# Kernel tuning notes

Hardware: AMD Instinct MI355X
Metric: run time of the kernel (lower is better)

## Reference

```python
import jax, jax.numpy as jnp
import numpy as np

POOL = 7  # adaptive_avg_pool2d output size (7,7)


def _bin_edges(start, length):
    """Adaptive-avg-pool bin boundaries.
    start, length: [N] int32 -> (lo, hi) each [N, POOL] absolute indices,
    matching torch: lo_i = floor(i*L/P), hi_i = ceil((i+1)*L/P).
    """
    i = jnp.arange(POOL, dtype=jnp.int32)
    lo = start[:, None] + (i[None, :] * length[:, None]) // POOL
    hi = start[:, None] + (-((-(i[None, :] + 1)) * length[:, None] // POOL))
    # note: ceil(a/b) = -(-a // b); written below explicitly
    hi = start[:, None] - ((-(i[None, :] + 1) * length[:, None]) // POOL)
    return lo, hi


def roi_adaptive_avg_pool(features, rois):
    """features: [1, C, H, W]; rois: [N, 4] int (x1,y1,x2,y2 inclusive).
    Returns [N, C, POOL, POOL] == torch stack of adaptive_avg_pool2d over
    features[:, :, y1:y2+1, x1:x2+1], vectorized via an integral image.
    """
    B, C, H, W = features.shape  # B == 1 (forced by shared_fcs input dim)
    # integral image with a zero row/col prepended: ii[y, x] = sum over [:y, :x]
    ii = jnp.cumsum(jnp.cumsum(features, axis=2), axis=3)
    ii = jnp.pad(ii, ((0, 0), (0, 0), (1, 0), (1, 0)))[0]  # [C, H+1, W+1]

    x1, y1, x2, y2 = rois[:, 0], rois[:, 1], rois[:, 2], rois[:, 3]
    ys, ye = _bin_edges(y1, y2 - y1 + 1)   # [N, POOL]
    xs, xe = _bin_edges(x1, x2 - x1 + 1)
    Y0, Y1 = ys[:, :, None], ye[:, :, None]   # [N, POOL, 1]
    X0, X1 = xs[:, None, :], xe[:, None, :]   # [N, 1, POOL]

    def gather(Y, X):
        return ii[:, Y, X]  # [C, N, POOL, POOL]

    sums = gather(Y1, X1) - gather(Y0, X1) - gather(Y1, X0) + gather(Y0, X0)
    area = ((Y1 - Y0) * (X1 - X0)).astype(features.dtype)  # [N, POOL, POOL]
    pooled = sums / area[None]                              # [C, N, POOL, POOL]
    return jnp.transpose(pooled, (1, 0, 2, 3))              # [N, C, POOL, POOL]


def setup_inputs() -> dict:
    key = jax.random.key(0)
    ks = jax.random.split(key, 12)
    C, H, W, N, F = 256, 336, 336, 2000, 256
    features = jax.random.normal(ks[0], (1, C, H, W), dtype=jnp.float32)
    # valid small ROIs (shuttlecock-sized), x1<=x2, y1<=y2, in-bounds
    x1 = jax.random.randint(ks[1], (N,), 0, W - 40)
    y1 = jax.random.randint(ks[2], (N,), 0, H - 40)
    bw = jax.random.randint(ks[3], (N,), 4, 40)
    bh = jax.random.randint(ks[4], (N,), 4, 40)
    rois = jnp.stack([x1, y1, jnp.minimum(x1 + bw, W - 1),
                      jnp.minimum(y1 + bh, H - 1)], axis=1).astype(jnp.int32)
    d_in = C * POOL * POOL
    w1 = jax.random.normal(ks[5], (d_in, F), dtype=jnp.float32) * (1.0 / np.sqrt(d_in))
    b1 = jnp.zeros((F,), dtype=jnp.float32)
    w2 = jax.random.normal(ks[6], (F, F), dtype=jnp.float32) * (1.0 / np.sqrt(F))
    b2 = jnp.zeros((F,), dtype=jnp.float32)
    w_cls = jax.random.normal(ks[7], (F, 2), dtype=jnp.float32) * 0.01
    b_cls = jnp.zeros((2,), dtype=jnp.float32)
    w_reg = jax.random.normal(ks[8], (F, 4), dtype=jnp.float32) * 0.001
    b_reg = jnp.zeros((4,), dtype=jnp.float32)
    return {"features": features, "rois": rois, "w1": w1, "b1": b1,
            "w2": w2, "b2": b2, "w_cls": w_cls, "b_cls": b_cls,
            "w_reg": w_reg, "b_reg": b_reg}


def reference(features, rois, w1, b1, w2, b2, w_cls, b_cls, w_reg, b_reg):
    roi_feats = roi_adaptive_avg_pool(features, rois)          # [N, C, 7, 7]
    roi_feats = roi_feats.reshape(roi_feats.shape[0], -1)      # [N, C*49]
    h = jax.nn.relu(roi_feats @ w1 + b1)
    h = jax.nn.relu(h @ w2 + b2)
    cls_score = h @ w_cls + b_cls                              # [N, num_classes+1]
    bbox_pred = h @ w_reg + b_reg                              # [N, 4]
    return (cls_score, bbox_pred)
```

## Files before the change

### kernel.cpp

```cpp
#include <hip/hip_runtime.h>

typedef unsigned int uint;
typedef unsigned short ushort;
typedef __bf16 v8bf __attribute__((ext_vector_type(8)));
typedef float v4f __attribute__((ext_vector_type(4)));
typedef float f2 __attribute__((ext_vector_type(2)));
typedef float f4v __attribute__((ext_vector_type(4)));

#define CCH 256
#define HH 336
#define WW 336
#define HWSZ (HH*WW)
#define NROI 2000
#define KDIM 12544
#define MPAD 2048
#define SPLITK 14
#define KSP (KDIM/SPLITK)

__device__ __forceinline__ ushort bf16r(float f) {
  uint u = __float_as_uint(f);
  u += 0x7fffu + ((u >> 16) & 1u);
  return (ushort)(u >> 16);
}
__device__ __forceinline__ uint packbf(float a, float b) {
  return (uint)bf16r(a) | ((uint)bf16r(b) << 16);
}

typedef const __attribute__((address_space(1))) uint* gas_t;
typedef __attribute__((address_space(3))) uint* las_t;
__device__ __forceinline__ void async16(const void* g, void* l) {
  __builtin_amdgcn_global_load_lds((gas_t)g, (las_t)l, 16, 0, 0);
}

#define GLOAD4(dst, ptr)                                             \
  asm volatile("global_load_dwordx4 %0, %1, off" : "=v"(dst) : "v"(ptr))

__global__ __launch_bounds__(256) void k_transpose(const float* __restrict__ f,
                                                   uint* __restrict__ ftu) {
  __shared__ uint T[64 * 128];
  int tid = threadIdx.x;
  int hw0 = blockIdx.x * 64;
  int hwq = tid & 15;
  int cp = tid >> 4;
  const float* base = f + hw0 + hwq * 4;
  f4v va[8], vb[8];
#pragma unroll
  for (int j = 0; j < 8; ++j) {
    int cpair = j * 16 + cp;
    const float* pa = base + (size_t)(2 * cpair) * HWSZ;
    GLOAD4(va[j], pa);
    GLOAD4(vb[j], pa + HWSZ);
  }
  asm volatile("s_waitcnt vmcnt(0)" ::: "memory");
  __builtin_amdgcn_sched_barrier(0);
  int sw = (hwq & 7) << 2;
#pragma unroll
  for (int j = 0; j < 8; ++j) {
    int cs = (j * 16 + cp) ^ sw;
    T[(hwq * 4 + 0) * 128 + cs] = packbf(va[j].x, vb[j].x);
    T[(hwq * 4 + 1) * 128 + cs] = packbf(va[j].y, vb[j].y);
    T[(hwq * 4 + 2) * 128 + cs] = packbf(va[j].z, vb[j].z);
    T[(hwq * 4 + 3) * 128 + cs] = packbf(va[j].w, vb[j].w);
  }
  __syncthreads();
  int co = tid & 31, r = tid >> 5;
#pragma unroll
  for (int i = 0; i < 8; ++i) {
    int row = i * 8 + r;
    int col = (co * 4) ^ (((row >> 2) & 7) << 2);
    uint4 v = *(const uint4*)&T[row * 128 + col];
    *(uint4*)(ftu + (size_t)(hw0 + row) * 128 + co * 4) = v;
  }
}

__global__ __launch_bounds__(256) void k_prep(const float* __restrict__ w1,
                                              uint* __restrict__ w1t_u,
                                              const float* __restrict__ w2,
                                              ushort* __restrict__ w2t,
                                              const int* __restrict__ rois,
                                              int* __restrict__ perm) {
  __shared__ ushort T[32][258];
  __shared__ int hist[64];
  __shared__ int keys[NROI];
  int tid = threadIdx.x;
  int b = blockIdx.x;
  if (b < 392) {
    int bin = b % 49;
    int c0 = (b / 49) * 32;
    int n = tid;
    for (int i = 0; i < 32; ++i)
      T[i][n] = bf16r(w1[(size_t)((c0 + i) * 49 + bin) * 256 + n]);
    __syncthreads();
    int cc = tid & 15;
    int nb = tid >> 4;
    for (int rep = 0; rep < 16; ++rep) {
      int nn = rep * 16 + nb;
      uint v = (uint)T[2 * cc][nn] | ((uint)T[2 * cc + 1][nn] << 16);
      w1t_u[(size_t)nn * (KDIM / 2) + bin * 128 + c0 / 2 + cc] = v;
    }
  } else if (b < 424) {
    int n = (b - 392) * 8 + (tid >> 5);
    for (int kl = 0; kl < 8; ++kl) {
      int k = kl * 32 + (tid & 31);
      w2t[n * 256 + k] = bf16r(w2[k * 256 + n]);
    }
  } else {
    if (tid < 64) hist[tid] = 0;
    __syncthreads();
    for (int i = tid; i < NROI; i += 256) {
      int x1 = rois[i * 4 + 0], y1 = rois[i * 4 + 1];
      int x2 = rois[i * 4 + 2], y2 = rois[i * 4 + 3];
      int cx = (x1 + x2) >> 1, cy = (y1 + y2) >> 1;
      int k = (cy / 42) * 8 + (cx / 42);
      keys[i] = k;
      atomicAdd(&hist[k], 1);
    }
    __syncthreads();
    if (tid < 64) {
      int v = hist[tid];
      int s = v;
#pragma unroll
      for (int d = 1; d < 64; d <<= 1) {
        int t2 = __shfl_up(s, d, 64);
        if (tid >= d) s += t2;
      }
      hist[tid] = s - v;
    }
    __syncthreads();
    for (int i = tid; i < NROI; i += 256) {
      int pos = atomicAdd(&hist[keys[i]], 1);
      perm[pos] = i;
    }
  }
}

__device__ __forceinline__ void pkacc(f2& acc, uint u) {
  f2 t;
  t.x = __uint_as_float(u << 16);
  t.y = __uint_as_float(u & 0xffff0000u);
  asm("v_pk_add_f32 %0, %1, %0" : "+v"(acc) : "v"(t));
}
#define UNPK2(S, u) do { pkacc(S[0], (u).x); pkacc(S[1], (u).y); } while (0)

#define GLOAD2(dst, ptr, OFF)                                        \
  asm volatile("global_load_dwordx2 %0, %1, off offset:" #OFF        \
               : "=v"(dst) : "v"(ptr))

template <int RH>
__device__ __forceinline__ void pool_unit(const uint2* __restrict__ ftu2,
                                          uint2* __restrict__ rfu2,
                                          int x1, int Lw, int ylo, int lane,
                                          uint ob) {
  const uint2* pr[RH];
#pragma unroll
  for (int r = 0; r < RH; ++r)
    pr[r] = ftu2 + (size_t)((ylo + r) * WW + x1) * 64 + lane;
  int xend = x1 + Lw;
  int b = 0;
  int lo_cur = x1;
  int hi_cur = x1 + (Lw + 6) / 7;
  int lo_next = x1 + Lw / 7;
  f2 P[2], Lc[2], Ln[2];
  P[0] = (f2){0.f, 0.f}; P[1] = (f2){0.f, 0.f};
  Lc[0] = (f2){0.f, 0.f}; Lc[1] = (f2){0.f, 0.f};
  Ln[0] = (f2){0.f, 0.f}; Ln[1] = (f2){0.f, 0.f};
  const float invr = 1.0f / (float)RH;
  for (int xc = x1; xc < xend; xc += 4) {
    uint2 v[4][RH];
#pragma unroll
    for (int r = 0; r < RH; ++r) {
      GLOAD2(v[0][r], pr[r], 0);
      GLOAD2(v[1][r], pr[r], 512);
      GLOAD2(v[2][r], pr[r], 1024);
      GLOAD2(v[3][r], pr[r], 1536);
    }
    asm volatile("s_waitcnt vmcnt(0)" ::: "memory");
    __builtin_amdgcn_sched_barrier(0);
#pragma unroll
    for (int r = 0; r < RH; ++r) pr[r] += 256;
#pragma unroll
    for (int c = 0; c < 4; ++c) {
      int x = xc + c;
      if (x < xend) {
#pragma unroll
        for (int r = 0; r < RH; ++r) UNPK2(P, v[c][r]);
        int xp = x + 1;
        if (xp == lo_next) { Ln[0] = P[0]; Ln[1] = P[1]; }
        while (b < 7 && xp == hi_cur) {
          float inv = invr / (float)(hi_cur - lo_cur);
          uint2 o;
          o.x = packbf((P[0].x - Lc[0].x) * inv, (P[0].y - Lc[0].y) * inv);
          o.y = packbf((P[1].x - Lc[1].x) * inv, (P[1].y - Lc[1].y) * inv);
          rfu2[ob + b * 64] = o;
          ++b;
          Lc[0] = Ln[0]; Lc[1] = Ln[1];
          lo_cur = lo_next;
          hi_cur = x1 + ((b + 1) * Lw + 6) / 7;
          lo_next = x1 + ((b + 1) * Lw) / 7;
          if (xp == lo_next) { Ln[0] = P[0]; Ln[1] = P[1]; }
        }
      }
    }
  }
}

__global__ __launch_bounds__(64) void k_pool(const int* __restrict__ rois,
                                             const int* __restrict__ perm,
                                             const uint2* __restrict__ ftu2,
                                             uint2* __restrict__ rfu2) {
  int L = blockIdx.x;
  int i = L >> 3;
  int slot = (L & 7) * 250 + i / 7;
  int by = i % 7;
  int n = perm[slot];
  int lane = threadIdx.x;
  int x1 = rois[n * 4 + 0], y1 = rois[n * 4 + 1];
  int x2 = rois[n * 4 + 2], y2 = rois[n * 4 + 3];
  int Lw = x2 - x1 + 1, Lh = y2 - y1 + 1;
  int ylo = y1 + (by * Lh) / 7;
  int yhi = y1 + ((by + 1) * Lh + 6) / 7;
  int rh = yhi - ylo;
  uint ob = ((uint)n * 49 + (uint)by * 7) * 64 + lane;
  switch (rh) {
    case 1: pool_unit<1>(ftu2, rfu2, x1, Lw, ylo, lane, ob); break;
    case 2: pool_unit<2>(ftu2, rfu2, x1, Lw, ylo, lane, ob); break;
    case 3: pool_unit<3>(ftu2, rfu2, x1, Lw, ylo, lane, ob); break;
    case 4: pool_unit<4>(ftu2, rfu2, x1, Lw, ylo, lane, ob); break;
    case 5: pool_unit<5>(ftu2, rfu2, x1, Lw, ylo, lane, ob); break;
    case 6: pool_unit<6>(ftu2, rfu2, x1, Lw, ylo, lane, ob); break;
    default: pool_unit<7>(ftu2, rfu2, x1, Lw, ylo, lane, ob); break;
  }
}

__global__ __launch_bounds__(256) void k_gemm1(const ushort* __restrict__ A,
                                               const ushort* __restrict__ B,
                                               float* __restrict__ P) {
  __shared__ ushort As[64 * 64];
  __shared__ ushort Bs[128 * 64];
  int m0 = blockIdx.x * 64;
  int n0 = blockIdx.y * 128;
  int ks = blockIdx.z;
  int k0 = ks * KSP;
  int tid = threadIdx.x;
  int lane = tid & 63, wv = tid >> 6;
  int wm = wv & 1, wn = wv >> 1;
  int lm = lane & 15, quad = lane >> 4;
  int srow = tid >> 3, scol = (tid & 7) * 8;
  v4f acc[2][4];
#pragma unroll
  for (int i = 0; i < 2; ++i)
#pragma unroll
    for (int j = 0; j < 4; ++j) acc[i][j] = (v4f){0.f, 0.f, 0.f, 0.f};
  const ushort* Ab = A + (size_t)(m0 + srow) * KDIM + k0 + scol;
  const ushort* Bb = B + (size_t)(n0 + srow) * KDIM + k0 + scol;
  for (int kt = 0; kt < KSP / 64; ++kt) {
    __syncthreads();
#pragma unroll
    for (int r = 0; r < 2; ++r)
      async16(Ab + (size_t)(r * 32) * KDIM + kt * 64, &As[(srow + r * 32) * 64 + scol]);
#pragma unroll
    for (int r = 0; r < 4; ++r)
      async16(Bb + (size_t)(r * 32) * KDIM + kt * 64, &Bs[(srow + r * 32) * 64 + scol]);
    __syncthreads();
#pragma unroll
    for (int kk = 0; kk < 64; kk += 32) {
      v8bf a[2], b[4];
#pragma unroll
      for (int i = 0; i < 2; ++i)
        a[i] = *(const v8bf*)&As[(wm * 32 + i * 16 + lm) * 64 + kk + quad * 8];
#pragma unroll
      for (int j = 0; j < 4; ++j)
        b[j] = *(const v8bf*)&Bs[(wn * 64 + j * 16 + lm) * 64 + kk + quad * 8];
#pragma unroll
      for (int i = 0; i < 2; ++i)
#pragma unroll
        for (int j = 0; j < 4; ++j)
          acc[i][j] = __builtin_amdgcn_mfma_f32_16x16x32_bf16(a[i], b[j], acc[i][j], 0, 0, 0);
    }
  }
  float* Pb = P + (size_t)ks * MPAD * 256;
#pragma unroll
  for (int i = 0; i < 2; ++i)
#pragma unroll
    for (int j = 0; j < 4; ++j) {
      int row = m0 + wm * 32 + i * 16 + quad * 4;
      int col = n0 + wn * 64 + j * 16 + lm;
#pragma unroll
      for (int r = 0; r < 4; ++r)
        Pb[(size_t)(row + r) * 256 + col] = acc[i][j][r];
    }
}

__global__ __launch_bounds__(256) void k_reduce(const float* __restrict__ P,
                                                const float* __restrict__ b1,
                                                uint* __restrict__ h1u) {
  int idx = blockIdx.x * 256 + threadIdx.x;
  int m = idx >> 7, np = idx & 127;
  const float2* Pp = (const float2*)P;
  float2 s = {0.f, 0.f};
#pragma unroll
  for (int ks = 0; ks < SPLITK; ++ks) {
    float2 v = Pp[(size_t)(ks * MPAD + m) * 128 + np];
    s.x += v.x; s.y += v.y;
  }
  s.x += b1[2 * np]; s.y += b1[2 * np + 1];
  s.x = fmaxf(s.x, 0.f); s.y = fmaxf(s.y, 0.f);
  h1u[idx] = packbf(s.x, s.y);
}

__global__ __launch_bounds__(256) void k_gemm2(const ushort* __restrict__ h1b,
                                               const ushort* __restrict__ w2t,
                                               const float* __restrict__ b2,
                                               const float* __restrict__ wcls,
                                               const float* __restrict__ bcls,
                                               const float* __restrict__ wreg,
                                               const float* __restrict__ breg,
                                               float* __restrict__ out) {
  __shared__ ushort As2[64 * 64];
  __shared__ ushort Bs2[256 * 64];
  __shared__ float Hs[64 * 257];
  int tid = threadIdx.x;
  int r0 = blockIdx.x * 64;
  int lane = tid & 63, wv = tid >> 6;
  int lm = lane & 15, quad = lane >> 4;
  int srow = tid >> 3, scol = (tid & 7) * 8;
  v4f acc[16];
#pragma unroll
  for (int j = 0; j < 16; ++j) acc[j] = (v4f){0.f, 0.f, 0.f, 0.f};
  for (int kt = 0; kt < 4; ++kt) {
    __syncthreads();
#pragma unroll
    for (int r = 0; r < 2; ++r)
      async16(h1b + (size_t)(r0 + srow + r * 32) * 256 + kt * 64 + scol,
              &As2[(srow + r * 32) * 64 + scol]);
#pragma unroll
    for (int r = 0; r < 8; ++r)
      async16(w2t + (size_t)(srow + r * 32) * 256 + kt * 64 + scol,
              &Bs2[(srow + r * 32) * 64 + scol]);
    __syncthreads();
#pragma unroll
    for (int kk = 0; kk < 64; kk += 32) {
      v8bf a = *(const v8bf*)&As2[(wv * 16 + lm) * 64 + kk + quad * 8];
#pragma unroll
      for (int j = 0; j < 16; ++j) {
        v8bf b = *(const v8bf*)&Bs2[(j * 16 + lm) * 64 + kk + quad * 8];
        acc[j] = __builtin_amdgcn_mfma_f32_16x16x32_bf16(a, b, acc[j], 0, 0, 0);
      }
    }
  }
#pragma unroll
  for (int j = 0; j < 16; ++j) {
    int nn = j * 16 + lm;
    float bb = b2[nn];
#pragma unroll
    for (int r = 0; r < 4; ++r) {
      int row = wv * 16 + quad * 4 + r;
      Hs[row * 257 + nn] = fmaxf(acc[j][r] + bb, 0.f);
    }
  }
  __syncthreads();
  for (int o = tid; o < 384; o += 256) {
    int hd = o >> 6, r = o & 63;
    int grow = r0 + r;
    float d = 0.f;
    if (hd < 2) {
      for (int k = 0; k < 256; ++k) d += Hs[r * 257 + k] * wcls[k * 2 + hd];
      d += bcls[hd];
      if (grow < NROI) out[grow * 2 + hd] = d;
    } else {
      int h4 = hd - 2;
      for (int k = 0; k < 256; ++k) d += Hs[r * 257 + k] * wreg[k * 4 + h4];
      d += breg[h4];
      if (grow < NROI) out[4000 + grow * 4 + h4] = d;
    }
  }
}

extern "C" void kernel_launch(void* const* d_in, const int* in_sizes, int n_in,
                              void* d_out, int out_size, void* d_ws, size_t ws_size,
                              hipStream_t stream) {
  const float* features = (const float*)d_in[0];
  const int* rois = (const int*)d_in[1];
  const float* w1 = (const float*)d_in[2];
  const float* b1 = (const float*)d_in[3];
  const float* w2 = (const float*)d_in[4];
  const float* b2 = (const float*)d_in[5];
  const float* wcls = (const float*)d_in[6];
  const float* bcls = (const float*)d_in[7];
  const float* wreg = (const float*)d_in[8];
  const float* breg = (const float*)d_in[9];
  char* ws = (char*)d_ws;
  ushort* ft  = (ushort*)(ws + 0);
  ushort* w1t = (ushort*)(ws + 57802752);
  ushort* w2t = (ushort*)(ws + 64225280);
  ushort* rf  = (ushort*)(ws + 64356352);
  int*    perm = (int*)(ws + 64356352 + (size_t)NROI * KDIM * 2);
  float*  P   = (float*)(ws + 115736576);
  ushort* h1b = (ushort*)(ws + 145096704);
  float* out = (float*)d_out;

  hipLaunchKernelGGL(k_transpose, dim3(HWSZ / 64), dim3(256), 0, stream,
                     features, (uint*)ft);
  hipLaunchKernelGGL(k_prep, dim3(425), dim3(256), 0, stream,
                     w1, (uint*)w1t, w2, w2t, rois, perm);
  hipLaunchKernelGGL(k_pool, dim3(NROI * 7), dim3(64), 0, stream, rois, perm,
                     (const uint2*)ft, (uint2*)rf);
  hipLaunchKernelGGL(k_gemm1, dim3(32, 2, SPLITK), dim3(256), 0, stream, rf, w1t, P);
  hipLaunchKernelGGL(k_reduce, dim3(1024), dim3(256), 0, stream, P, b1, (uint*)h1b);
  hipLaunchKernelGGL(k_gemm2, dim3(32), dim3(256), 0, stream, h1b, w2t, b2, wcls, bcls, wreg, breg, out);
}
```

Baseline: 332.4 us.

## Merge transpose with prep, fold split-K reduction into gemm2, halve split-K

Fuses the feature transpose and weight/ROI prep kernels into one launch, and moves the split-K partial-sum reduction plus bias/ReLU/bf16 pack into the gemm2 prologue. The H1 tile now lives in swizzled LDS instead of a global round trip. SPLITK drops from 14 to 7 to reduce partial-sum traffic. The trade-offs are fewer blocks in gemm1 (less parallelism) and only 32 blocks doing the reduction inside gemm2, plus more LDS per gemm2 block.

```diff
diff --git a/kernel.cpp b/kernel.cpp
--- a/kernel.cpp
+++ b/kernel.cpp
@@ -14,8 +14,9 @@
 #define NROI 2000
 #define KDIM 12544
 #define MPAD 2048
-#define SPLITK 14
+#define SPLITK 7
 #define KSP (KDIM/SPLITK)
+#define NTRB (HWSZ/64)
 
 __device__ __forceinline__ ushort bf16r(float f) {
   uint u = __float_as_uint(f);
@@ -35,56 +36,55 @@
 #define GLOAD4(dst, ptr)                                             \
   asm volatile("global_load_dwordx4 %0, %1, off" : "=v"(dst) : "v"(ptr))
 
-__global__ __launch_bounds__(256) void k_transpose(const float* __restrict__ f,
-                                                   uint* __restrict__ ftu) {
-  __shared__ uint T[64 * 128];
+__global__ __launch_bounds__(256) void k_trprep(const float* __restrict__ f,
+                                                uint* __restrict__ ftu,
+                                                const float* __restrict__ w1,
+                                                uint* __restrict__ w1t_u,
+                                                const float* __restrict__ w2,
+                                                ushort* __restrict__ w2t,
+                                                const int* __restrict__ rois,
+                                                int* __restrict__ perm) {
+  __shared__ uint SM[64 * 128];
   int tid = threadIdx.x;
-  int hw0 = blockIdx.x * 64;
-  int hwq = tid & 15;
-  int cp = tid >> 4;
-  const float* base = f + hw0 + hwq * 4;
-  f4v va[8], vb[8];
-#pragma unroll
-  for (int j = 0; j < 8; ++j) {
-    int cpair = j * 16 + cp;
-    const float* pa = base + (size_t)(2 * cpair) * HWSZ;
-    GLOAD4(va[j], pa);
-    GLOAD4(vb[j], pa + HWSZ);
-  }
-  asm volatile("s_waitcnt vmcnt(0)" ::: "memory");
-  __builtin_amdgcn_sched_barrier(0);
-  int sw = (hwq & 7) << 2;
-#pragma unroll
-  for (int j = 0; j < 8; ++j) {
-    int cs = (j * 16 + cp) ^ sw;
-    T[(hwq * 4 + 0) * 128 + cs] = packbf(va[j].x, vb[j].x);
-    T[(hwq * 4 + 1) * 128 + cs] = packbf(va[j].y, vb[j].y);
-    T[(hwq * 4 + 2) * 128 + cs] = packbf(va[j].z, vb[j].z);
-    T[(hwq * 4 + 3) * 128 + cs] = packbf(va[j].w, vb[j].w);
-  }
-  __syncthreads();
-  int co = tid & 31, r = tid >> 5;
-#pragma unroll
-  for (int i = 0; i < 8; ++i) {
-    int row = i * 8 + r;
-    int col = (co * 4) ^ (((row >> 2) & 7) << 2);
-    uint4 v = *(const uint4*)&T[row * 128 + col];
-    *(uint4*)(ftu + (size_t)(hw0 + row) * 128 + co * 4) = v;
-  }
-}
-
-__global__ __launch_bounds__(256) void k_prep(const float* __restrict__ w1,
-                                              uint* __restrict__ w1t_u,
-                                              const float* __restrict__ w2,
-                                              ushort* __restrict__ w2t,
-                                              const int* __restrict__ rois,
-                                              int* __restrict__ perm) {
-  __shared__ ushort T[32][258];
-  __shared__ int hist[64];
-  __shared__ int keys[NROI];
-  int tid = threadIdx.x;
-  int b = blockIdx.x;
+  if (blockIdx.x < NTRB) {
+    uint* T = SM;
+    int hw0 = blockIdx.x * 64;
+    int hwq = tid & 15;
+    int cp = tid >> 4;
+    const float* base = f + hw0 + hwq * 4;
+    f4v va[8], vb[8];
+#pragma unroll
+    for (int j = 0; j < 8; ++j) {
+      int cpair = j * 16 + cp;
+      const float* pa = base + (size_t)(2 * cpair) * HWSZ;
+      GLOAD4(va[j], pa);
+      GLOAD4(vb[j], pa + HWSZ);
+    }
+    asm volatile("s_waitcnt vmcnt(0)" ::: "memory");
+    __builtin_amdgcn_sched_barrier(0);
+    int sw = (hwq & 7) << 2;
+#pragma unroll
+    for (int j = 0; j < 8; ++j) {
+      int cs = (j * 16 + cp) ^ sw;
+      T[(hwq * 4 + 0) * 128 + cs] = packbf(va[j].x, vb[j].x);
+      T[(hwq * 4 + 1) * 128 + cs] = packbf(va[j].y, vb[j].y);
+      T[(hwq * 4 + 2) * 128 + cs] = packbf(va[j].z, vb[j].z);
+      T[(hwq * 4 + 3) * 128 + cs] = packbf(va[j].w, vb[j].w);
+    }
+    __syncthreads();
+    int co = tid & 31, r = tid >> 5;
+#pragma unroll
+    for (int i = 0; i < 8; ++i) {
+      int row = i * 8 + r;
+      int col = (co * 4) ^ (((row >> 2) & 7) << 2);
+      uint4 v = *(const uint4*)&T[row * 128 + col];
+      *(uint4*)(ftu + (size_t)(hw0 + row) * 128 + co * 4) = v;
+    }
+    return;
+  }
+  int b = blockIdx.x - NTRB;
   if (b < 392) {
+    ushort (*T)[258] = reinterpret_cast<ushort (*)[258]>(SM);
     int bin = b % 49;
     int c0 = (b / 49) * 32;
     int n = tid;
@@ -105,6 +105,8 @@
       w2t[n * 256 + k] = bf16r(w2[k * 256 + n]);
     }
   } else {
+    int* hist = (int*)((char*)SM + 16512);
+    int* keys = hist + 64;
     if (tid < 64) hist[tid] = 0;
     __syncthreads();
     for (int i = tid; i < NROI; i += 256) {
@@ -291,24 +293,8 @@
     }
 }
 
-__global__ __launch_bounds__(256) void k_reduce(const float* __restrict__ P,
-                                                const float* __restrict__ b1,
-                                                uint* __restrict__ h1u) {
-  int idx = blockIdx.x * 256 + threadIdx.x;
-  int m = idx >> 7, np = idx & 127;
-  const float2* Pp = (const float2*)P;
-  float2 s = {0.f, 0.f};
-#pragma unroll
-  for (int ks = 0; ks < SPLITK; ++ks) {
-    float2 v = Pp[(size_t)(ks * MPAD + m) * 128 + np];
-    s.x += v.x; s.y += v.y;
-  }
-  s.x += b1[2 * np]; s.y += b1[2 * np + 1];
-  s.x = fmaxf(s.x, 0.f); s.y = fmaxf(s.y, 0.f);
-  h1u[idx] = packbf(s.x, s.y);
-}
-
-__global__ __launch_bounds__(256) void k_gemm2(const ushort* __restrict__ h1b,
+__global__ __launch_bounds__(256) void k_gemm2(const float* __restrict__ P,
+                                               const float* __restrict__ b1,
                                                const ushort* __restrict__ w2t,
                                                const float* __restrict__ b2,
                                                const float* __restrict__ wcls,
@@ -316,7 +302,7 @@
                                                const float* __restrict__ wreg,
                                                const float* __restrict__ breg,
                                                float* __restrict__ out) {
-  __shared__ ushort As2[64 * 64];
+  __shared__ ushort HsA[64 * 256];
   __shared__ ushort Bs2[256 * 64];
   __shared__ float Hs[64 * 257];
   int tid = threadIdx.x;
@@ -324,15 +310,34 @@
   int lane = tid & 63, wv = tid >> 6;
   int lm = lane & 15, quad = lane >> 4;
   int srow = tid >> 3, scol = (tid & 7) * 8;
+  uint* H = (uint*)HsA;
+  for (int it = 0; it < 16; ++it) {
+    int e = it * 256 + tid;
+    int row = e >> 6;
+    int c4 = e & 63;
+    float4 s = {0.f, 0.f, 0.f, 0.f};
+#pragma unroll
+    for (int ks = 0; ks < SPLITK; ++ks) {
+      float4 v = ((const float4*)P)[((size_t)ks * MPAD + r0 + row) * 64 + c4];
+      s.x += v.x; s.y += v.y; s.z += v.z; s.w += v.w;
+    }
+    int col = c4 * 4;
+    s.x = fmaxf(s.x + b1[col + 0], 0.f);
+    s.y = fmaxf(s.y + b1[col + 1], 0.f);
+    s.z = fmaxf(s.z + b1[col + 2], 0.f);
+    s.w = fmaxf(s.w + b1[col + 3], 0.f);
+    int cs = (c4 >> 1) ^ (row & 7);
+    int ui = row * 128 + cs * 4 + (c4 & 1) * 2;
+    H[ui]     = packbf(s.x, s.y);
+    H[ui + 1] = packbf(s.z, s.w);
+  }
   v4f acc[16];
 #pragma unroll
   for (int j = 0; j < 16; ++j) acc[j] = (v4f){0.f, 0.f, 0.f, 0.f};
+  int arow = wv * 16 + lm;
+  int asw = (arow & 7) << 3;
   for (int kt = 0; kt < 4; ++kt) {
     __syncthreads();
-#pragma unroll
-    for (int r = 0; r < 2; ++r)
-      async16(h1b + (size_t)(r0 + srow + r * 32) * 256 + kt * 64 + scol,
-              &As2[(srow + r * 32) * 64 + scol]);
 #pragma unroll
     for (int r = 0; r < 8; ++r)
       async16(w2t + (size_t)(srow + r * 32) * 256 + kt * 64 + scol,
@@ -340,7 +345,7 @@
     __syncthreads();
 #pragma unroll
     for (int kk = 0; kk < 64; kk += 32) {
-      v8bf a = *(const v8bf*)&As2[(wv * 16 + lm) * 64 + kk + quad * 8];
+      v8bf a = *(const v8bf*)&HsA[arow * 256 + ((kt * 64 + kk + quad * 8) ^ asw)];
 #pragma unroll
       for (int j = 0; j < 16; ++j) {
         v8bf b = *(const v8bf*)&Bs2[(j * 16 + lm) * 64 + kk + quad * 8];
@@ -396,16 +401,13 @@
   ushort* rf  = (ushort*)(ws + 64356352);
   int*    perm = (int*)(ws + 64356352 + (size_t)NROI * KDIM * 2);
   float*  P   = (float*)(ws + 115736576);
-  ushort* h1b = (ushort*)(ws + 145096704);
   float* out = (float*)d_out;
 
-  hipLaunchKernelGGL(k_transpose, dim3(HWSZ / 64), dim3(256), 0, stream,
-                     features, (uint*)ft);
-  hipLaunchKernelGGL(k_prep, dim3(425), dim3(256), 0, stream,
-                     w1, (uint*)w1t, w2, w2t, rois, perm);
+  hipLaunchKernelGGL(k_trprep, dim3(NTRB + 425), dim3(256), 0, stream,
+                     features, (uint*)ft, w1, (uint*)w1t, w2, w2t, rois, perm);
   hipLaunchKernelGGL(k_pool, dim3(NROI * 7), dim3(64), 0, stream, rois, perm,
                      (const uint2*)ft, (uint2*)rf);
   hipLaunchKernelGGL(k_gemm1, dim3(32, 2, SPLITK), dim3(256), 0, stream, rf, w1t, P);
-  hipLaunchKernelGGL(k_reduce, dim3(1024), dim3(256), 0, stream, P, b1, (uint*)h1b);
-  hipLaunchKernelGGL(k_gemm2, dim3(32), dim3(256), 0, stream, h1b, w2t, b2, wcls, bcls, wreg, breg, out);
-}
+  hipLaunchKernelGGL(k_gemm2, dim3(32), dim3(256), 0, stream, P, b1, w2t, b2,
+                     wcls, bcls, wreg, breg, out);
+}
```

Measured after the change: 331.0 us. About the same (-0.4%).
